# Kernel tuning notes

Hardware: AMD Instinct MI355X
Metric: run time of the kernel (lower is better)

Reference implementation:

```python
import jax, jax.numpy as jnp
import numpy as np

N_HEADS = 16

def setup_inputs() -> dict:
    key = jax.random.key(0)
    k1, k2, k3, k4, k5 = jax.random.split(key, 5)
    B, S, D = 2, 2048, 1024
    x = jax.random.normal(k1, (B, S, D), dtype=jnp.float32)
    # parameters scaled ~ fan-in to keep softmax logits sane
    w_in = jax.random.normal(k2, (D, 3 * D), dtype=jnp.float32) * (1.0 / np.sqrt(D))
    b_in = jax.random.normal(k3, (3 * D,), dtype=jnp.float32) * 0.02
    w_out = jax.random.normal(k4, (D, D), dtype=jnp.float32) * (1.0 / np.sqrt(D))
    b_out = jax.random.normal(k5, (D,), dtype=jnp.float32) * 0.02
    return {"x": x, "w_in": w_in, "b_in": b_in, "w_out": w_out, "b_out": b_out,
            "causal_mask": 1}


def reference(x, w_in, b_in, w_out, b_out, causal_mask):
    B, S, D = x.shape
    H = N_HEADS
    dh = D // H
    qkv = x @ w_in + b_in                        # [B, S, 3D]
    q, k, v = jnp.split(qkv, 3, axis=-1)          # each [B, S, D]
    q = q.reshape(B, S, H, dh)
    k = k.reshape(B, S, H, dh)
    v = v.reshape(B, S, H, dh)
    # scores: [B, H, Sq, Sk]
    scores = jnp.einsum("bqhd,bkhd->bhqk", q, k)
    if causal_mask:
        mask = jnp.triu(jnp.ones((S, S), dtype=bool), k=1)
        scores = jnp.where(mask, -jnp.inf, scores)
    scores = scores / jnp.sqrt(jnp.asarray(dh, dtype=scores.dtype))
    weight = jax.nn.softmax(scores, axis=-1)
    out = jnp.einsum("bhqk,bkhd->bqhd", weight, v).reshape(B, S, D)
    return out @ w_out + b_out
```

## Files before the change

kernel.cpp:

```cpp
#include <hip/hip_runtime.h>
#include <hip/hip_bf16.h>

typedef __attribute__((ext_vector_type(8))) short short8;
typedef __attribute__((ext_vector_type(4))) short s16x4;
typedef __attribute__((ext_vector_type(4))) float f32x4;
typedef unsigned short u16;

__device__ inline u16 f2bf(float f) {
    union { float f; unsigned u; } x{f};
    unsigned r = (x.u + 0x7fff + ((x.u >> 16) & 1)) >> 16;
    return (u16)r;
}

__device__ inline unsigned pkbf(float hi, float lo) {
    unsigned a = __builtin_bit_cast(unsigned, hi) + 0x8000u;
    unsigned b = __builtin_bit_cast(unsigned, lo) + 0x8000u;
    return __builtin_amdgcn_perm(a, b, 0x07060302u);
}

__device__ inline void glds16(const u16* g, u16* l) {
    __builtin_amdgcn_global_load_lds(
        (const __attribute__((address_space(1))) void*)g,
        (__attribute__((address_space(3))) void*)l, 16, 0, 0);
}

__global__ __launch_bounds__(256) void prep(const float* __restrict__ x,
                                            const float* __restrict__ w_in,
                                            const float* __restrict__ w_out,
                                            u16* __restrict__ Xb,
                                            u16* __restrict__ WtIn,
                                            u16* __restrict__ WtOut) {
    __shared__ float tile[32][33];
    int bx = blockIdx.x, tid = threadIdx.x;
    if (bx < 4096) {
        int i = (bx * 256 + tid) * 4;
        float4 v = *(const float4*)&x[i];
        uint2 o;
        o.x = (unsigned)f2bf(v.x) | ((unsigned)f2bf(v.y) << 16);
        o.y = (unsigned)f2bf(v.z) | ((unsigned)f2bf(v.w) << 16);
        *(uint2*)&Xb[i] = o;
        return;
    }
    const float* W; u16* Wt; int K, N, n0, k0;
    if (bx < 7168) {
        int b2 = bx - 4096;
        W = w_in; Wt = WtIn; K = 1024; N = 3072;
        n0 = (b2 % 96) * 32; k0 = (b2 / 96) * 32;
    } else {
        int b3 = bx - 7168;
        W = w_out; Wt = WtOut; K = 1024; N = 1024;
        n0 = (b3 & 31) * 32; k0 = (b3 >> 5) * 32;
    }
    int tx = tid & 31, ty = tid >> 5;
    for (int i = 0; i < 32; i += 8)
        tile[ty + i][tx] = W[(size_t)(k0 + ty + i) * N + n0 + tx];
    __syncthreads();
    for (int i = 0; i < 32; i += 8)
        Wt[(size_t)(n0 + ty + i) * K + k0 + tx] = f2bf(tile[tx][ty + i]);
}

#define BK 64
template<int TBM, int TBN>
__global__ __launch_bounds__(256) void gemm_bt(const u16* __restrict__ A,
                                               const u16* __restrict__ Bt,
                                               const float* __restrict__ bias,
                                               void* __restrict__ C,
                                               int M, int N, int K, int c_is_f32,
                                               int qcols, float qscale,
                                               u16* __restrict__ vt, int vcol0) {
    __shared__ u16 smem[TBM * BK + TBN * BK + 2048];
    u16* As = smem;
    u16* Bs = smem + TBM * BK;

    int tid = threadIdx.x;
    int wave = tid >> 6, lane = tid & 63;
    int quad = lane >> 4, l16 = lane & 15;
    int wm = (wave >> 1) * (TBM / 2), wn = (wave & 1) * (TBN / 2);
    constexpr int MI = TBM / 32, NJ = TBN / 32;

    int nm = M / TBM, nn = N / TBN;
    const int GM = 8;
    int per_group = GM * nn;
    int group = blockIdx.x / per_group;
    int rem = blockIdx.x % per_group;
    int first_m = group * GM;
    int gsz = (nm - first_m < GM) ? (nm - first_m) : GM;
    int m0 = (first_m + rem % gsz) * TBM;
    int n0 = (rem / gsz) * TBN;

    f32x4 acc[MI][NJ] = {};

    for (int k0 = 0; k0 < K; k0 += BK) {
        __syncthreads();
        for (int i = 0; i < TBM * 8 / 256; i++) {
            int c = tid + i * 256;
            int r = c >> 3, cc = c & 7;
            int gsrc = (cc ^ (r & 7)) * 8;
            glds16(&A[(size_t)(m0 + r) * K + k0 + gsrc], As + c * 8);
        }
        for (int i = 0; i < TBN * 8 / 256; i++) {
            int c = tid + i * 256;
            int r = c >> 3, cc = c & 7;
            int gsrc = (cc ^ (r & 7)) * 8;
            glds16(&Bt[(size_t)(n0 + r) * K + k0 + gsrc], Bs + c * 8);
        }
        __syncthreads();
        for (int ks = 0; ks < 2; ks++) {
            short8 af[MI], bf[NJ];
            for (int i = 0; i < MI; i++) {
                int row = wm + i * 16 + l16;
                int slot = (ks * 4 + quad) ^ (row & 7);
                af[i] = *(short8*)&As[row * BK + slot * 8];
            }
            for (int j = 0; j < NJ; j++) {
                int row = wn + j * 16 + l16;
                int slot = (ks * 4 + quad) ^ (row & 7);
                bf[j] = *(short8*)&Bs[row * BK + slot * 8];
            }
            for (int i = 0; i < MI; i++)
                for (int j = 0; j < NJ; j++)
                    acc[i][j] = __builtin_amdgcn_mfma_f32_16x16x32_bf16(
                        af[i], bf[j], acc[i][j], 0, 0, 0);
        }
    }

    if (c_is_f32) {
        for (int i = 0; i < MI; i++)
            for (int j = 0; j < NJ; j++) {
                int col = n0 + wn + j * 16 + l16;
                float bv = bias ? bias[col] : 0.f;
                for (int r = 0; r < 4; r++) {
                    int row = m0 + wm + i * 16 + quad * 4 + r;
                    ((float*)C)[(size_t)row * N + col] = acc[i][j][r] + bv;
                }
            }
    } else {
        __syncthreads();
        u16 (*buf)[136] = (u16(*)[136])smem;
        for (int i = 0; i < MI; i++)
            for (int j = 0; j < NJ; j++) {
                int col = wn + j * 16 + l16;
                float bv = bias ? bias[n0 + col] : 0.f;
                float scl = (n0 + col < qcols) ? qscale : 1.f;
                for (int r = 0; r < 4; r++)
                    buf[wm + i * 16 + quad * 4 + r][col] =
                        f2bf((acc[i][j][r] + bv) * scl);
            }
        __syncthreads();
        u16* Cb = (u16*)C;
        for (int it = 0; it < TBM * 16 / 256; it++) {
            int c = tid + it * 256;
            int row = c / (TBN / 8), k8 = c % (TBN / 8);
            uint4 v = *(uint4*)&buf[row][k8 * 8];
            *(uint4*)&Cb[(size_t)(m0 + row) * N + n0 + k8 * 8] = v;
        }
        if (vt && n0 >= vcol0) {
            int b = m0 >> 11, s0 = m0 & 2047;
            int hbase = (n0 - vcol0) >> 6;
            for (int pass = 0; pass < TBN / 16; pass++) {
                int col = pass * 16 + (tid >> 4);
                int so = (tid & 15) * 8;
                alignas(16) u16 tmp[8];
                for (int r = 0; r < 8; r++) tmp[r] = buf[so + r][col];
                int h = hbase + (col >> 6), dh = col & 63;
                *(uint4*)&vt[(size_t)((b * 16 + h) * 64 + dh) * 2048 + s0 + so] =
                    __builtin_bit_cast(uint4, tmp);
            }
        }
    }
}

__global__ __launch_bounds__(256, 2) void attn_kernel(const u16* __restrict__ qkv,
                                                      const u16* __restrict__ VT,
                                                      u16* __restrict__ out) {
    const int S = 2048, D = 1024, stride = 3072;
    int idx = blockIdx.x;
    int slot = idx >> 8;
    int r5 = idx & 255;
    int p = r5 >> 5, bh = r5 & 31;
    int qt = slot ? p : 15 - p;
    int b = bh >> 4, h = bh & 15;
    int tid = threadIdx.x;
    int wave = tid >> 6, lane = tid & 63;
    int quad = lane >> 4, l16 = lane & 15;

    __shared__ u16 Klds[2][2][64 * 64];
    __shared__ u16 Vlds[2][2][64 * 64];

    const u16* Qp = qkv + (size_t)(b * S) * stride + h * 64;
    const u16* Kp = Qp + D;
    const u16* Vtp = VT + (size_t)bh * 64 * S;

    short8 qf[2][2];
    for (int qh = 0; qh < 2; qh++) {
        int qrow = qt * 128 + wave * 32 + qh * 16 + l16;
        qf[qh][0] = *(const short8*)&Qp[(size_t)qrow * stride + quad * 8];
        qf[qh][1] = *(const short8*)&Qp[(size_t)qrow * stride + 32 + quad * 8];
    }

    auto stage = [&](int kt, int bsel, int ch) {
        for (int i = 0; i < 2; i++) {
            int c = tid + i * 256;
            int rr = c >> 3, cc = c & 7;
            int gsrc = (cc ^ (rr & 7)) * 8;
            glds16(&Kp[(size_t)(kt * 64 + rr) * stride + gsrc],
                   &Klds[bsel][ch][c * 8]);
            glds16(&Vtp[(size_t)rr * S + kt * 64 + gsrc],
                   &Vlds[bsel][ch][c * 8]);
        }
    };

    stage(0, 0, 0);
    stage(1, 0, 1);

    f32x4 O[4][2] = {};
    float ls[2] = {0.f, 0.f};

    int np = qt + 1;
    for (int j = 0; j < np; j++) {
        int cur = j & 1;
        __syncthreads();
        if (j + 1 < np) {
            stage(2 * (j + 1), cur ^ 1, 0);
            stage(2 * (j + 1) + 1, cur ^ 1, 1);
        }
        bool last = (j == qt);

        auto qk = [&](int ch, f32x4 st[2][4]) {
            short8 kf[4][2];
            for (int nb = 0; nb < 4; nb++) {
                int rr = nb * 16 + l16;
                int s0 = ((0 + quad) ^ (rr & 7)) * 8;
                int s1 = ((4 + quad) ^ (rr & 7)) * 8;
                kf[nb][0] = *(short8*)&Klds[cur][ch][rr * 64 + s0];
                kf[nb][1] = *(short8*)&Klds[cur][ch][rr * 64 + s1];
            }
            for (int qh = 0; qh < 2; qh++)
                for (int nb = 0; nb < 4; nb++) {
                    f32x4 t = {};
                    t = __builtin_amdgcn_mfma_f32_16x16x32_bf16(
                        kf[nb][0], qf[qh][0], t, 0, 0, 0);
                    t = __builtin_amdgcn_mfma_f32_16x16x32_bf16(
                        kf[nb][1], qf[qh][1], t, 0, 0, 0);
                    st[qh][nb] = t;
                }
        };
        auto sm = [&](int ch, f32x4 st[2][4], s16x4 pfc[2][4]) {
            for (int qh = 0; qh < 2; qh++) {
                if (last) {
                    int qabs = qt * 128 + wave * 32 + qh * 16 + l16;
                    for (int nb = 0; nb < 4; nb++) {
                        int kb0 = (2 * j + ch) * 64 + nb * 16 + quad * 4;
                        for (int r = 0; r < 4; r++) {
                            float e = __builtin_amdgcn_exp2f(st[qh][nb][r]);
                            st[qh][nb][r] = (kb0 + r <= qabs) ? e : 0.f;
                        }
                    }
                } else {
                    for (int nb = 0; nb < 4; nb++)
                        for (int r = 0; r < 4; r++)
                            st[qh][nb][r] = __builtin_amdgcn_exp2f(st[qh][nb][r]);
                }
                for (int nb = 0; nb < 4; nb++) {
                    ls[qh] += (st[qh][nb][0] + st[qh][nb][1]) +
                              (st[qh][nb][2] + st[qh][nb][3]);
                    uint2 pk;
                    pk.x = pkbf(st[qh][nb][1], st[qh][nb][0]);
                    pk.y = pkbf(st[qh][nb][3], st[qh][nb][2]);
                    pfc[qh][nb] = __builtin_bit_cast(s16x4, pk);
                }
            }
        };
        auto pv = [&](int ch, s16x4 pfc[2][4]) {
            for (int db = 0; db < 4; db++) {
                int rr = db * 16 + l16;
                for (int kc = 0; kc < 4; kc++) {
                    int g = kc * 2 + (quad >> 1);
                    int sl = g ^ (rr & 7);
                    int off = rr * 64 + sl * 8 + (quad & 1) * 4;
                    s16x4 vf = *(s16x4*)&Vlds[cur][ch][off];
                    for (int qh = 0; qh < 2; qh++)
                        O[db][qh] = __builtin_amdgcn_mfma_f32_16x16x16bf16_1k(
                            vf, pfc[qh][kc], O[db][qh], 0, 0, 0);
                }
            }
        };

        f32x4 stA[2][4], stB[2][4];
        s16x4 pfA[2][4], pfB[2][4];

        __builtin_amdgcn_s_setprio(1);
        qk(0, stA);
        __builtin_amdgcn_s_setprio(0);
        sm(0, stA, pfA);
        __builtin_amdgcn_s_setprio(1);
        qk(1, stB);
        pv(0, pfA);
        __builtin_amdgcn_s_setprio(0);
        sm(1, stB, pfB);
        __builtin_amdgcn_s_setprio(1);
        pv(1, pfB);
        __builtin_amdgcn_s_setprio(0);
    }

    for (int qh = 0; qh < 2; qh++) {
        float v = ls[qh];
        v += __shfl_xor(v, 16);
        v += __shfl_xor(v, 32);
        float rinv = 1.f / v;
        int qrow = qt * 128 + wave * 32 + qh * 16 + l16;
        for (int db = 0; db < 4; db++) {
            uint2 o;
            o.x = pkbf(O[db][qh][1] * rinv, O[db][qh][0] * rinv);
            o.y = pkbf(O[db][qh][3] * rinv, O[db][qh][2] * rinv);
            *(uint2*)&out[(size_t)(b * S + qrow) * D + h * 64 + db * 16 +
                          quad * 4] = o;
        }
    }
}

extern "C" void kernel_launch(void* const* d_in, const int* in_sizes, int n_in,
                              void* d_out, int out_size, void* d_ws, size_t ws_size,
                              hipStream_t stream) {
    const float* x     = (const float*)d_in[0];
    const float* w_in  = (const float*)d_in[1];
    const float* b_in  = (const float*)d_in[2];
    const float* w_out = (const float*)d_in[3];
    const float* b_out = (const float*)d_in[4];

    const int Bsz = 2, S = 2048, D = 1024, H = 16;
    const int M = Bsz * S;
    const int N1 = 3 * D;
    const float sc = 0.125f * 1.44269504f;

    u16* ws    = (u16*)d_ws;
    u16* Xb    = ws;
    u16* WtIn  = Xb + (size_t)M * D;
    u16* WtOut = WtIn + (size_t)N1 * D;
    u16* qkvb  = WtOut + (size_t)D * D;
    u16* attnb = qkvb + (size_t)M * N1;
    u16* Vt    = attnb + (size_t)M * D;

    prep<<<8192, 256, 0, stream>>>(x, w_in, w_out, Xb, WtIn, WtOut);
    gemm_bt<128, 128><<<(M / 128) * (N1 / 128), 256, 0, stream>>>(
        Xb, WtIn, b_in, qkvb, M, N1, D, 0, D, sc, Vt, 2048);
    attn_kernel<<<512, 256, 0, stream>>>(qkvb, Vt, attnb);
    gemm_bt<64, 128><<<(M / 64) * (D / 128), 256, 0, stream>>>(
        attnb, WtOut, b_out, d_out, M, D, D, 1, 0, 1.f, nullptr, 1 << 30);
}
```

Before: 173.3 us.

## Add dedicated 256x256-tile QKV GEMM with phased double-buffered LDS loads

Replaces the generic 128x128 QKV projection GEMM with a specialized 256x256-tile, 512-thread kernel. It double-buffers K-tiles in LDS, splits global-to-LDS loads into four phases that are interleaved with the MFMA work, and raises wave priority around the MFMAs. The epilogue writes through an LDS buffer for coalesced stores and emits the transposed V. Bigger tiles cut global traffic per flop, but the grid drops to 192 blocks, which may underfill the CUs. The 128KB of LDS per block also limits occupancy.

```diff
diff --git a/kernel.cpp b/kernel.cpp
--- a/kernel.cpp
+++ b/kernel.cpp
@@ -57,6 +57,118 @@
     __syncthreads();
     for (int i = 0; i < 32; i += 8)
         Wt[(size_t)(n0 + ty + i) * K + k0 + tx] = f2bf(tile[tx][ty + i]);
+}
+
+__global__ __launch_bounds__(512, 2) void gemm1_256(const u16* __restrict__ A,
+                                                    const u16* __restrict__ Bt,
+                                                    const float* __restrict__ bias,
+                                                    u16* __restrict__ C,
+                                                    u16* __restrict__ vt,
+                                                    float qscale) {
+    __shared__ u16 smem[2][2][256 * 64];
+    int tid = threadIdx.x;
+    int wave = tid >> 6, lane = tid & 63;
+    int quad = lane >> 4, l16 = lane & 15;
+    int wm = (wave >> 2) * 128, wn = (wave & 3) * 64;
+    int bn = blockIdx.x % 12, bm = blockIdx.x / 12;
+    int m0 = bm * 256, n0 = bn * 256;
+
+    auto stage_phase = [&](int kt, int s, int p) {
+        int k0 = kt * 64;
+        int op = p >> 1;
+        int row0 = (p & 1) * 128;
+        const u16* G = op ? Bt : A;
+        int base0 = op ? n0 : m0;
+        u16* dst = &smem[s][op][0];
+        #pragma unroll
+        for (int i = 0; i < 2; i++) {
+            int c = tid + i * 512;
+            int r = row0 + (c >> 3), cc = c & 7;
+            int gsrc = (cc ^ (r & 7)) * 8;
+            glds16(&G[(size_t)(base0 + r) * 1024 + k0 + gsrc],
+                   dst + row0 * 64 + c * 8);
+        }
+    };
+
+    #pragma unroll
+    for (int p = 0; p < 4; p++) stage_phase(0, 0, p);
+    __syncthreads();
+
+    f32x4 acc[8][4] = {};
+
+    for (int kt = 0; kt < 16; kt++) {
+        int s = kt & 1;
+        const u16* As = &smem[s][0][0];
+        const u16* Bs = &smem[s][1][0];
+
+        short8 bfr[4][2];
+        #pragma unroll
+        for (int j = 0; j < 4; j++) {
+            int row = wn + j * 16 + l16;
+            bfr[j][0] = *(short8*)&Bs[row * 64 + ((0 + quad) ^ (row & 7)) * 8];
+            bfr[j][1] = *(short8*)&Bs[row * 64 + ((4 + quad) ^ (row & 7)) * 8];
+        }
+        #pragma unroll
+        for (int p = 0; p < 4; p++) {
+            short8 afr[2][2];
+            #pragma unroll
+            for (int ii = 0; ii < 2; ii++) {
+                int row = wm + (p * 2 + ii) * 16 + l16;
+                afr[ii][0] = *(short8*)&As[row * 64 + ((0 + quad) ^ (row & 7)) * 8];
+                afr[ii][1] = *(short8*)&As[row * 64 + ((4 + quad) ^ (row & 7)) * 8];
+            }
+            if (kt + 1 < 16) stage_phase(kt + 1, s ^ 1, p);
+            __builtin_amdgcn_s_barrier();
+            __builtin_amdgcn_s_setprio(1);
+            #pragma unroll
+            for (int ii = 0; ii < 2; ii++)
+                #pragma unroll
+                for (int j = 0; j < 4; j++)
+                    #pragma unroll
+                    for (int ks = 0; ks < 2; ks++)
+                        acc[p * 2 + ii][j] = __builtin_amdgcn_mfma_f32_16x16x32_bf16(
+                            afr[ii][ks], bfr[j][ks], acc[p * 2 + ii][j], 0, 0, 0);
+            __builtin_amdgcn_s_setprio(0);
+            __builtin_amdgcn_s_barrier();
+        }
+        __syncthreads();
+    }
+
+    float scl = (n0 < 1024) ? qscale : 1.f;
+    u16* buf = &smem[0][0][0];
+    #pragma unroll
+    for (int i = 0; i < 8; i++)
+        #pragma unroll
+        for (int j = 0; j < 4; j++) {
+            int col = wn + j * 16 + l16;
+            float bv = bias[n0 + col];
+            #pragma unroll
+            for (int r = 0; r < 4; r++) {
+                int row = wm + i * 16 + quad * 4 + r;
+                buf[row * 256 + col] = f2bf((acc[i][j][r] + bv) * scl);
+            }
+        }
+    __syncthreads();
+    for (int it = 0; it < 16; it++) {
+        int c = tid + it * 512;
+        int row = c >> 5, k8 = c & 31;
+        uint4 v = *(uint4*)&buf[row * 256 + k8 * 8];
+        *(uint4*)&C[(size_t)(m0 + row) * 3072 + n0 + k8 * 8] = v;
+    }
+    if (n0 >= 2048) {
+        int b = m0 >> 11, s0 = m0 & 2047;
+        int hbase = (n0 - 2048) >> 6;
+        for (int pass = 0; pass < 16; pass++) {
+            int col = pass * 16 + (tid >> 5);
+            int so = (tid & 31) * 8;
+            alignas(16) u16 tmp[8];
+            #pragma unroll
+            for (int r = 0; r < 8; r++) tmp[r] = buf[(so + r) * 256 + col];
+            int h = hbase + (col >> 6), dh = col & 63;
+            *(uint4*)&vt[(size_t)((b * 16 + h) * 64 + dh) * 2048 + s0 + so] =
+                __builtin_bit_cast(uint4, tmp);
+        }
+    }
 }
 
 #define BK 64
@@ -342,8 +454,8 @@
     u16* Vt    = attnb + (size_t)M * D;
 
     prep<<<8192, 256, 0, stream>>>(x, w_in, w_out, Xb, WtIn, WtOut);
-    gemm_bt<128, 128><<<(M / 128) * (N1 / 128), 256, 0, stream>>>(
-        Xb, WtIn, b_in, qkvb, M, N1, D, 0, D, sc, Vt, 2048);
+    gemm1_256<<<(M / 256) * (N1 / 256), 512, 0, stream>>>(
+        Xb, WtIn, b_in, qkvb, Vt, sc);
     attn_kernel<<<512, 256, 0, stream>>>(qkvb, Vt, attnb);
     gemm_bt<64, 128><<<(M / 64) * (D / 128), 256, 0, stream>>>(
         attnb, WtOut, b_out, d_out, M, D, D, 1, 0, 1.f, nullptr, 1 << 30);
```

After: 199.6 us. +15.2%, slower.

## Split attention KV range across two blocks and combine partials in separate kernel

Applied to the files above, without the earlier changes.

Each query tile's key range is split into two halves processed by separate blocks (1024 blocks instead of 512), each writing unnormalized fp32 partial outputs and row sums to workspace. A new combine kernel sums the halves, normalizes and writes bf16. LDS is halved to single 64-key tiles and launch bounds rise to 4 blocks per CU to increase occupancy. This adds an extra launch and fp32 partial traffic, and removes the two-chunk softmax/PV interleaving within an iteration.

```diff
diff --git a/kernel.cpp b/kernel.cpp
--- a/kernel.cpp
+++ b/kernel.cpp
@@ -170,22 +170,25 @@
     }
 }
 
-__global__ __launch_bounds__(256, 2) void attn_kernel(const u16* __restrict__ qkv,
+__global__ __launch_bounds__(256, 4) void attn_kernel(const u16* __restrict__ qkv,
                                                       const u16* __restrict__ VT,
-                                                      u16* __restrict__ out) {
+                                                      float* __restrict__ Op,
+                                                      float* __restrict__ lp) {
     const int S = 2048, D = 1024, stride = 3072;
     int idx = blockIdx.x;
-    int slot = idx >> 8;
-    int r5 = idx & 255;
-    int p = r5 >> 5, bh = r5 & 31;
+    int half = idx >> 9;
+    int r9 = idx & 511;
+    int slot = r9 >> 8;
+    int r8 = r9 & 255;
+    int p = r8 >> 5, bh = r8 & 31;
     int qt = slot ? p : 15 - p;
     int b = bh >> 4, h = bh & 15;
     int tid = threadIdx.x;
     int wave = tid >> 6, lane = tid & 63;
     int quad = lane >> 4, l16 = lane & 15;
 
-    __shared__ u16 Klds[2][2][64 * 64];
-    __shared__ u16 Vlds[2][2][64 * 64];
+    __shared__ u16 Klds[2][64 * 64];
+    __shared__ u16 Vlds[2][64 * 64];
 
     const u16* Qp = qkv + (size_t)(b * S) * stride + h * 64;
     const u16* Kp = Qp + D;
@@ -198,124 +201,129 @@
         qf[qh][1] = *(const short8*)&Qp[(size_t)qrow * stride + 32 + quad * 8];
     }
 
-    auto stage = [&](int kt, int bsel, int ch) {
+    auto stage = [&](int kt, int bsel) {
         for (int i = 0; i < 2; i++) {
             int c = tid + i * 256;
             int rr = c >> 3, cc = c & 7;
             int gsrc = (cc ^ (rr & 7)) * 8;
             glds16(&Kp[(size_t)(kt * 64 + rr) * stride + gsrc],
-                   &Klds[bsel][ch][c * 8]);
+                   &Klds[bsel][c * 8]);
             glds16(&Vtp[(size_t)rr * S + kt * 64 + gsrc],
-                   &Vlds[bsel][ch][c * 8]);
+                   &Vlds[bsel][c * 8]);
         }
     };
 
-    stage(0, 0, 0);
-    stage(1, 0, 1);
+    int k0t = half * (qt + 1);
+    int k1t = k0t + (qt + 1);
+    stage(k0t, 0);
 
     f32x4 O[4][2] = {};
     float ls[2] = {0.f, 0.f};
 
-    int np = qt + 1;
-    for (int j = 0; j < np; j++) {
-        int cur = j & 1;
-        __syncthreads();
-        if (j + 1 < np) {
-            stage(2 * (j + 1), cur ^ 1, 0);
-            stage(2 * (j + 1) + 1, cur ^ 1, 1);
-        }
-        bool last = (j == qt);
-
-        auto qk = [&](int ch, f32x4 st[2][4]) {
-            short8 kf[4][2];
+    for (int kt = k0t; kt < k1t; kt++) {
+        int cur = (kt - k0t) & 1;
+        __syncthreads();
+        if (kt + 1 < k1t) stage(kt + 1, cur ^ 1);
+        bool maskt = (kt >= 2 * qt);
+
+        short8 kf[4][2];
+        for (int nb = 0; nb < 4; nb++) {
+            int rr = nb * 16 + l16;
+            kf[nb][0] = *(short8*)&Klds[cur][rr * 64 + ((0 + quad) ^ (rr & 7)) * 8];
+            kf[nb][1] = *(short8*)&Klds[cur][rr * 64 + ((4 + quad) ^ (rr & 7)) * 8];
+        }
+        f32x4 st[2][4];
+        __builtin_amdgcn_s_setprio(1);
+        for (int qh = 0; qh < 2; qh++)
             for (int nb = 0; nb < 4; nb++) {
-                int rr = nb * 16 + l16;
-                int s0 = ((0 + quad) ^ (rr & 7)) * 8;
-                int s1 = ((4 + quad) ^ (rr & 7)) * 8;
-                kf[nb][0] = *(short8*)&Klds[cur][ch][rr * 64 + s0];
-                kf[nb][1] = *(short8*)&Klds[cur][ch][rr * 64 + s1];
-            }
-            for (int qh = 0; qh < 2; qh++)
+                f32x4 t = {};
+                t = __builtin_amdgcn_mfma_f32_16x16x32_bf16(
+                    kf[nb][0], qf[qh][0], t, 0, 0, 0);
+                t = __builtin_amdgcn_mfma_f32_16x16x32_bf16(
+                    kf[nb][1], qf[qh][1], t, 0, 0, 0);
+                st[qh][nb] = t;
+            }
+        __builtin_amdgcn_s_setprio(0);
+
+        s16x4 pf[2][4];
+        for (int qh = 0; qh < 2; qh++) {
+            if (maskt) {
+                int qabs = qt * 128 + wave * 32 + qh * 16 + l16;
                 for (int nb = 0; nb < 4; nb++) {
-                    f32x4 t = {};
-                    t = __builtin_amdgcn_mfma_f32_16x16x32_bf16(
-                        kf[nb][0], qf[qh][0], t, 0, 0, 0);
-                    t = __builtin_amdgcn_mfma_f32_16x16x32_bf16(
-                        kf[nb][1], qf[qh][1], t, 0, 0, 0);
-                    st[qh][nb] = t;
+                    int kb0 = kt * 64 + nb * 16 + quad * 4;
+                    for (int r = 0; r < 4; r++) {
+                        float e = __builtin_amdgcn_exp2f(st[qh][nb][r]);
+                        st[qh][nb][r] = (kb0 + r <= qabs) ? e : 0.f;
+                    }
                 }
-        };
-        auto sm = [&](int ch, f32x4 st[2][4], s16x4 pfc[2][4]) {
-            for (int qh = 0; qh < 2; qh++) {
-                if (last) {
-                    int qabs = qt * 128 + wave * 32 + qh * 16 + l16;
-                    for (int nb = 0; nb < 4; nb++) {
-                        int kb0 = (2 * j + ch) * 64 + nb * 16 + quad * 4;
-                        for (int r = 0; r < 4; r++) {
-                            float e = __builtin_amdgcn_exp2f(st[qh][nb][r]);
-                            st[qh][nb][r] = (kb0 + r <= qabs) ? e : 0.f;
-                        }
-                    }
-                } else {
-                    for (int nb = 0; nb < 4; nb++)
-                        for (int r = 0; r < 4; r++)
-                            st[qh][nb][r] = __builtin_amdgcn_exp2f(st[qh][nb][r]);
-                }
-                for (int nb = 0; nb < 4; nb++) {
-                    ls[qh] += (st[qh][nb][0] + st[qh][nb][1]) +
-                              (st[qh][nb][2] + st[qh][nb][3]);
-                    uint2 pk;
-                    pk.x = pkbf(st[qh][nb][1], st[qh][nb][0]);
-                    pk.y = pkbf(st[qh][nb][3], st[qh][nb][2]);
-                    pfc[qh][nb] = __builtin_bit_cast(s16x4, pk);
-                }
-            }
-        };
-        auto pv = [&](int ch, s16x4 pfc[2][4]) {
-            for (int db = 0; db < 4; db++) {
-                int rr = db * 16 + l16;
-                for (int kc = 0; kc < 4; kc++) {
-                    int g = kc * 2 + (quad >> 1);
-                    int sl = g ^ (rr & 7);
-                    int off = rr * 64 + sl * 8 + (quad & 1) * 4;
-                    s16x4 vf = *(s16x4*)&Vlds[cur][ch][off];
-                    for (int qh = 0; qh < 2; qh++)
-                        O[db][qh] = __builtin_amdgcn_mfma_f32_16x16x16bf16_1k(
-                            vf, pfc[qh][kc], O[db][qh], 0, 0, 0);
-                }
-            }
-        };
-
-        f32x4 stA[2][4], stB[2][4];
-        s16x4 pfA[2][4], pfB[2][4];
+            } else {
+                for (int nb = 0; nb < 4; nb++)
+                    for (int r = 0; r < 4; r++)
+                        st[qh][nb][r] = __builtin_amdgcn_exp2f(st[qh][nb][r]);
+            }
+            for (int nb = 0; nb < 4; nb++) {
+                ls[qh] += (st[qh][nb][0] + st[qh][nb][1]) +
+                          (st[qh][nb][2] + st[qh][nb][3]);
+                uint2 pk;
+                pk.x = pkbf(st[qh][nb][1], st[qh][nb][0]);
+                pk.y = pkbf(st[qh][nb][3], st[qh][nb][2]);
+                pf[qh][nb] = __builtin_bit_cast(s16x4, pk);
+            }
+        }
 
         __builtin_amdgcn_s_setprio(1);
-        qk(0, stA);
+        for (int db = 0; db < 4; db++) {
+            int rr = db * 16 + l16;
+            for (int kc = 0; kc < 4; kc++) {
+                int g = kc * 2 + (quad >> 1);
+                int sl = g ^ (rr & 7);
+                int off = rr * 64 + sl * 8 + (quad & 1) * 4;
+                s16x4 vf = *(s16x4*)&Vlds[cur][off];
+                for (int qh = 0; qh < 2; qh++)
+                    O[db][qh] = __builtin_amdgcn_mfma_f32_16x16x16bf16_1k(
+                        vf, pf[qh][kc], O[db][qh], 0, 0, 0);
+            }
+        }
         __builtin_amdgcn_s_setprio(0);
-        sm(0, stA, pfA);
-        __builtin_amdgcn_s_setprio(1);
-        qk(1, stB);
-        pv(0, pfA);
-        __builtin_amdgcn_s_setprio(0);
-        sm(1, stB, pfB);
-        __builtin_amdgcn_s_setprio(1);
-        pv(1, pfB);
-        __builtin_amdgcn_s_setprio(0);
-    }
-
+    }
+
+    int e = (bh * 16 + qt) * 2 + half;
+    float* Ope = Op + (size_t)e * (128 * 64);
     for (int qh = 0; qh < 2; qh++) {
         float v = ls[qh];
         v += __shfl_xor(v, 16);
         v += __shfl_xor(v, 32);
-        float rinv = 1.f / v;
-        int qrow = qt * 128 + wave * 32 + qh * 16 + l16;
-        for (int db = 0; db < 4; db++) {
-            uint2 o;
-            o.x = pkbf(O[db][qh][1] * rinv, O[db][qh][0] * rinv);
-            o.y = pkbf(O[db][qh][3] * rinv, O[db][qh][2] * rinv);
-            *(uint2*)&out[(size_t)(b * S + qrow) * D + h * 64 + db * 16 +
-                          quad * 4] = o;
-        }
+        if (lane < 16)
+            lp[e * 128 + wave * 32 + qh * 16 + lane] = v;
+        int row = wave * 32 + qh * 16 + l16;
+        for (int db = 0; db < 4; db++)
+            *(f32x4*)&Ope[row * 64 + db * 16 + quad * 4] = O[db][qh];
+    }
+}
+
+__global__ __launch_bounds__(256) void combine(const float* __restrict__ Op,
+                                               const float* __restrict__ lp,
+                                               u16* __restrict__ out) {
+    int cb = blockIdx.x;
+    int bh = cb & 31, qt = cb >> 5;
+    int b = bh >> 4, h = bh & 15;
+    int tid = threadIdx.x;
+    int row = tid >> 1, c0 = (tid & 1) * 32;
+    int e = (bh * 16 + qt) * 2;
+    float l = lp[e * 128 + row] + lp[(e + 1) * 128 + row];
+    float rinv = 1.f / l;
+    const float* p0 = Op + (size_t)e * (128 * 64) + row * 64 + c0;
+    const float* p1 = p0 + 128 * 64;
+    u16* po = out + ((size_t)(b * 2048 + qt * 128 + row)) * 1024 + h * 64 + c0;
+    for (int d = 0; d < 32; d += 8) {
+        f32x4 a0 = *(const f32x4*)&p0[d], a1 = *(const f32x4*)&p0[d + 4];
+        f32x4 b0 = *(const f32x4*)&p1[d], b1 = *(const f32x4*)&p1[d + 4];
+        uint4 o;
+        o.x = pkbf((a0[1] + b0[1]) * rinv, (a0[0] + b0[0]) * rinv);
+        o.y = pkbf((a0[3] + b0[3]) * rinv, (a0[2] + b0[2]) * rinv);
+        o.z = pkbf((a1[1] + b1[1]) * rinv, (a1[0] + b1[0]) * rinv);
+        o.w = pkbf((a1[3] + b1[3]) * rinv, (a1[2] + b1[2]) * rinv);
+        *(uint4*)&po[d] = o;
     }
 }
 
@@ -340,11 +348,14 @@
     u16* qkvb  = WtOut + (size_t)D * D;
     u16* attnb = qkvb + (size_t)M * N1;
     u16* Vt    = attnb + (size_t)M * D;
+    float* Op  = (float*)(Vt + (size_t)Bsz * H * 64 * S);
+    float* lp  = Op + (size_t)1024 * 128 * 64;
 
     prep<<<8192, 256, 0, stream>>>(x, w_in, w_out, Xb, WtIn, WtOut);
     gemm_bt<128, 128><<<(M / 128) * (N1 / 128), 256, 0, stream>>>(
         Xb, WtIn, b_in, qkvb, M, N1, D, 0, D, sc, Vt, 2048);
-    attn_kernel<<<512, 256, 0, stream>>>(qkvb, Vt, attnb);
+    attn_kernel<<<1024, 256, 0, stream>>>(qkvb, Vt, Op, lp);
+    combine<<<512, 256, 0, stream>>>(Op, lp, attnb);
     gemm_bt<64, 128><<<(M / 64) * (D / 128), 256, 0, stream>>>(
         attnb, WtOut, b_out, d_out, M, D, D, 1, 0, 1.f, nullptr, 1 << 30);
 }
```

Result: slower. 210.9 us (+21.7%).
